# Performance work log

Hardware: AMD Instinct MI355X
Metric: run time of the kernel (lower is better)

Reference implementation:

```python
import jax, jax.numpy as jnp
import numpy as np

B, T, D, F, E = 4, 2048, 1024, 2048, 16  # batch, seq, hidden, intermediate, experts


def setup_inputs() -> dict:
    key = jax.random.key(0)
    k0, k1, k2, k3 = jax.random.split(key, 4)
    x = jax.random.normal(k0, (B, T, D), dtype=jnp.float32)
    # gate: torch Linear(D, E, bias=False); store as [D, E] so logits = h @ Wg
    Wg = jax.random.normal(k1, (D, E), dtype=jnp.float32) * 0.02
    # experts: kaiming_uniform(a=sqrt(5)) -> U(-1/sqrt(fan_in), 1/sqrt(fan_in))
    W1 = jax.random.uniform(k2, (E, D, F), minval=-1.0, maxval=1.0, dtype=jnp.float32) / np.sqrt(D)
    W2 = jax.random.uniform(k3, (E, F, D), minval=-1.0, maxval=1.0, dtype=jnp.float32) / np.sqrt(F)
    return {"x": x, "Wg": Wg, "W1": W1, "W2": W2}


def reference(x, Wg, W1, W2):
    b, t, d = x.shape
    e = Wg.shape[1]
    h = x.reshape(-1, d)                     # [N, D], N = b*t tokens
    n = h.shape[0]

    # --- gate: top-2 routing with fp32 softmax over the 2 selected logits ---
    logits = h @ Wg                          # [N, E]
    scores, idx = jax.lax.top_k(logits, 2)   # [N, 2]
    scores = jax.nn.softmax(scores.astype(jnp.float32), axis=-1).astype(x.dtype)

    # dense combine weights [N, E]: weight of expert e for each token (0 if not routed)
    combine = jnp.zeros((n, e), dtype=x.dtype).at[
        jnp.arange(n)[:, None], idx
    ].add(scores)

    # --- dispatch/combine: scan over experts, weight-accumulate outputs ---
    # Mathematically identical to the masked-loop original: tokens not routed
    # to expert e contribute with weight 0.
    def step(acc, params):
        W1e, W2e, w = params                  # [D,F], [F,D], [N]
        out = jax.nn.silu(h @ W1e) @ W2e      # [N, D]
        return acc + w[:, None] * out, None

    y, _ = jax.lax.scan(step, jnp.zeros_like(h), (W1, W2, combine.T))
    return y.reshape(b, t, d)
```

## Files before the change

### kernel.cpp

```cpp
#include <hip/hip_runtime.h>
#include <hip/hip_bf16.h>

#define NTOK 8192
#define DDIM 1024
#define FDIM 2048
#define NEXP 16
#define CAP   1280
#define CAPRG 80

#define WS_COUNTS 0
#define WS_TOKL   4096
#define WS_WGTL   (4096 + NTOK*NEXP*4)
#define WS_POS    (4096 + 2*NTOK*NEXP*4)
#define WS_TW     (4096 + 2*NTOK*NEXP*4 + NTOK*8)
#define WS2_XG   (size_t)(2u<<20)
#define WS2_W1   (size_t)(42u<<20)
#define WS2_W2   (size_t)(106u<<20)
#define WS2_UG   (size_t)(170u<<20)

typedef short bf16x8 __attribute__((ext_vector_type(8)));
typedef float f32x4  __attribute__((ext_vector_type(4)));

__device__ __forceinline__ unsigned short f2bf(float f) {
  unsigned int u = __builtin_bit_cast(unsigned int, f);
  u += 0x7fffu + ((u >> 16) & 1u);
  return (unsigned short)(u >> 16);
}
__device__ __forceinline__ unsigned int pk2(float a, float b) {
  return (unsigned int)f2bf(a) | ((unsigned int)f2bf(b) << 16);
}
__device__ __forceinline__ float bf2f(unsigned int u) {
  return __builtin_bit_cast(float, u << 16);
}
__device__ __forceinline__ float silu_f(float s) {
  return s / (1.f + __expf(-s));
}
__device__ __forceinline__ void gld_lds16(const void* g, void* l) {
  __builtin_amdgcn_global_load_lds((const __attribute__((address_space(1))) void*)g,
                                   (__attribute__((address_space(3))) void*)l, 16, 0, 0);
}

__global__ __launch_bounds__(1024) void gate_kernel(
    const float* __restrict__ x, const float* __restrict__ Wg,
    int* __restrict__ counts, int* __restrict__ tokl, float* __restrict__ wgtl,
    int* __restrict__ pos, float* __restrict__ tw) {
  __shared__ float WgT[NEXP][DDIM];
  __shared__ int   se[32];
  __shared__ float swt[32];
  __shared__ int   sbase[16];
  int tid = threadIdx.x;
#pragma unroll
  for (int i = 0; i < 4; ++i) {
    int i4 = i * 1024 + tid;
    float4 v = ((const float4*)Wg)[i4];
    int k = i4 >> 2;
    int e0 = (i4 * 4) & 15;
    WgT[e0][k] = v.x; WgT[e0 + 1][k] = v.y;
    WgT[e0 + 2][k] = v.z; WgT[e0 + 3][k] = v.w;
  }
  __syncthreads();

  int wid = tid >> 6, lane = tid & 63;
  int tok = blockIdx.x * 16 + wid;
  const float* xr = x + (size_t)tok * DDIM;
  float xv[16];
#pragma unroll
  for (int j = 0; j < 16; ++j) xv[j] = xr[lane + 64 * j];
  float lg[NEXP];
#pragma unroll
  for (int e = 0; e < NEXP; ++e) {
    float s = 0.f;
#pragma unroll
    for (int j = 0; j < 16; ++j) s += xv[j] * WgT[e][lane + 64 * j];
#pragma unroll
    for (int off = 32; off > 0; off >>= 1) s += __shfl_xor(s, off);
    lg[e] = s;
  }
  int e0 = 0; float b0 = lg[0];
#pragma unroll
  for (int e = 1; e < NEXP; ++e) if (lg[e] > b0) { b0 = lg[e]; e0 = e; }
  int e1 = -1; float b1 = -3.4e38f;
#pragma unroll
  for (int e = 0; e < NEXP; ++e) if (e != e0 && lg[e] > b1) { b1 = lg[e]; e1 = e; }
  float t = expf(b1 - b0);
  float w0 = 1.f / (1.f + t);
  float w1 = t / (1.f + t);
  if (lane == 0) {
    se[wid * 2] = e0;  swt[wid * 2] = w0;
    se[wid * 2 + 1] = e1;  swt[wid * 2 + 1] = w1;
  }
  __syncthreads();

  if (tid < 16) {
    int cnt = 0;
#pragma unroll
    for (int i = 0; i < 32; ++i) cnt += (se[i] == tid) ? 1 : 0;
    sbase[tid] = cnt ? atomicAdd(&counts[tid * 16], cnt) : 0;
    int slot = sbase[tid];
    for (int i = 0; i < 32; ++i) {
      if (se[i] == tid) {
        int tk = blockIdx.x * 16 + (i >> 1);
        float w = swt[i];
        if (slot < CAP) { tokl[tid * NTOK + slot] = tk; wgtl[tid * NTOK + slot] = w; }
        pos[tk * 2 + (i & 1)] = (slot < CAP) ? (tid * CAP + slot) : -1;
        tw[tk * 2 + (i & 1)] = w;
        slot++;
      }
    }
  }
}

__global__ __launch_bounds__(256) void convert_w2(
    const float* __restrict__ W1, const float* __restrict__ W2,
    unsigned short* __restrict__ W1s, unsigned short* __restrict__ W2s) {
  __shared__ float tile[32][133];
  int b = blockIdx.x;
  bool isw2 = b >= 8192;
  int bb = isw2 ? b - 8192 : b;
  int e = bb >> 9;
  int r = bb & 511;
  int t = threadIdx.x;
  const float* src;
  int kk, cb, C;
  if (!isw2) {
    kk = r >> 4; cb = r & 15; C = FDIM;
    src = W1 + ((size_t)e << 21) + (size_t)(kk * 32) * FDIM + cb * 128;
  } else {
    kk = r >> 3; cb = r & 7; C = DDIM;
    src = W2 + ((size_t)e << 21) + (size_t)(kk * 32) * DDIM + cb * 128;
  }
  int c4 = (t & 31) * 4, rr0 = t >> 5;
#pragma unroll
  for (int rd = 0; rd < 4; ++rd) {
    int rr = rr0 + rd * 8;
    float4 v = *(const float4*)(src + (size_t)rr * C + c4);
    tile[rr][c4] = v.x; tile[rr][c4 + 1] = v.y;
    tile[rr][c4 + 2] = v.z; tile[rr][c4 + 3] = v.w;
  }
  __syncthreads();
  int w = t >> 6, lane = t & 63, llo = lane & 15, lhi = lane >> 4;
#pragma unroll
  for (int u = 0; u < 2; ++u) {
    int c2 = w * 2 + u;
    float v[8];
#pragma unroll
    for (int j = 0; j < 8; ++j) {
      int row = isw2 ? (4 * lhi + (j & 3) + 16 * (j >> 2)) : (lhi * 8 + j);
      v[j] = tile[row][c2 * 16 + llo];
    }
    uint4 o;
    o.x = pk2(v[0], v[1]); o.y = pk2(v[2], v[3]);
    o.z = pk2(v[4], v[5]); o.w = pk2(v[6], v[7]);
    size_t gid = isw2 ? (((size_t)e * 64 + kk) * 64 + (cb * 8 + c2))
                      : (((size_t)e * 128 + (cb * 8 + c2)) * 32 + kk);
    *(uint4*)((isw2 ? W2s : W1s) + (gid << 9) + lane * 8) = o;
  }
}

__global__ __launch_bounds__(512) void gather_x(
    const float* __restrict__ x, const int* __restrict__ counts,
    const int* __restrict__ tokl, unsigned short* __restrict__ Xg) {
  int chunk = blockIdx.x * 8 + (threadIdx.x >> 6);
  int lane = threadIdx.x & 63, llo = lane & 15, lhi = lane >> 4;
  int kb = chunk & 31;
  int rg = (chunk >> 5) % CAPRG;
  int e = chunk / (CAPRG * 32);
  int cnt = min(counts[e * 16], CAP);
  int slot = rg * 16 + llo;
  uint4 o = {0u, 0u, 0u, 0u};
  if (slot < cnt) {
    int tok = tokl[e * NTOK + slot];
    const float* p = x + (size_t)tok * DDIM + kb * 32 + lhi * 8;
    float4 a = *(const float4*)p, b2 = *(const float4*)(p + 4);
    o.x = pk2(a.x, a.y); o.y = pk2(a.z, a.w);
    o.z = pk2(b2.x, b2.y); o.w = pk2(b2.z, b2.w);
  }
  *(uint4*)(Xg + ((size_t)chunk << 9) + lane * 8) = o;
}

__global__ __launch_bounds__(512, 2) void g1(
    const unsigned short* __restrict__ W1s, const unsigned short* __restrict__ Xg,
    const int* __restrict__ counts, unsigned short* __restrict__ Ug) {
  int id = blockIdx.x;
  int xcd = id & 7, q = id >> 3;
  int r = q / 40, s = q % 40;
  int e = xcd * 2 + r;
  int ft = s & 7;
  int tt = s >> 3;
  int cnt = min(counts[e * 16], CAP);
  if (tt * 256 >= cnt) return;

  extern __shared__ char smem[];
  int tid = threadIdx.x, wid = tid >> 6, lane = tid & 63;
  int llo = lane & 15, lhi = lane >> 4;
  int wm = wid >> 2, wn = wid & 3;

  f32x4 acc[8][4];
#pragma unroll
  for (int i = 0; i < 8; ++i)
#pragma unroll
    for (int j = 0; j < 4; ++j) acc[i][j] = (f32x4){0.f, 0.f, 0.f, 0.f};

  const size_t abase = ((size_t)e * 128 + ft * 16) * 32;
  const size_t bbase = ((size_t)e * CAPRG + tt * 16) * 32;

#define G1_STAGE(B, T)                                                          \
  {                                                                             \
    char* dst = smem + (B) * 65536;                                             \
    _Pragma("unroll")                                                           \
    for (int i = 0; i < 8; ++i) {                                               \
      int c = wid * 8 + i;                                                      \
      if (c < 32) {                                                             \
        int fl = c >> 1, kkl = c & 1;                                           \
        gld_lds16(W1s + ((abase + (size_t)fl * 32 + (T) * 2 + kkl) << 9) + lane * 8, \
                  dst + c * 1024);                                              \
      } else {                                                                  \
        int cb = c - 32, rgl = cb >> 1, kkl = cb & 1;                           \
        gld_lds16(Xg + ((bbase + (size_t)rgl * 32 + (T) * 2 + kkl) << 9) + lane * 8, \
                  dst + c * 1024);                                              \
      }                                                                         \
    }                                                                           \
  }

  G1_STAGE(0, 0);
  int cur = 0;
  for (int t = 0; t < 16; ++t) {
    if (t < 15) {
      G1_STAGE(cur ^ 1, t + 1);
      asm volatile("s_waitcnt vmcnt(8)" ::: "memory");
    } else {
      asm volatile("s_waitcnt vmcnt(0)" ::: "memory");
    }
    __builtin_amdgcn_s_barrier();
    const char* bufc = smem + cur * 65536;
#pragma unroll
    for (int kk = 0; kk < 2; ++kk) {
      bf16x8 af[8], bx[4];
#pragma unroll
      for (int fi = 0; fi < 8; ++fi)
        af[fi] = *(const bf16x8*)(bufc + (((wm * 8 + fi) * 2 + kk) << 10) + lane * 16);
#pragma unroll
      for (int ti = 0; ti < 4; ++ti)
        bx[ti] = *(const bf16x8*)(bufc + 32768 + (((wn * 4 + ti) * 2 + kk) << 10) + lane * 16);
#pragma unroll
      for (int fi = 0; fi < 8; ++fi)
#pragma unroll
        for (int ti = 0; ti < 4; ++ti)
          acc[fi][ti] = __builtin_amdgcn_mfma_f32_16x16x32_bf16(af[fi], bx[ti], acc[fi][ti], 0, 0, 0);
    }
    asm volatile("s_waitcnt lgkmcnt(0)" ::: "memory");
    __builtin_amdgcn_s_barrier();
    cur ^= 1;
  }

#pragma unroll
  for (int ti = 0; ti < 4; ++ti) {
    int rg = tt * 16 + wn * 4 + ti;
#pragma unroll
    for (int p = 0; p < 4; ++p) {
      int fo = ft * 8 + wm * 4 + p;
      uint4 v;
      v.x = pk2(silu_f(acc[2 * p][ti][0]), silu_f(acc[2 * p][ti][1]));
      v.y = pk2(silu_f(acc[2 * p][ti][2]), silu_f(acc[2 * p][ti][3]));
      v.z = pk2(silu_f(acc[2 * p + 1][ti][0]), silu_f(acc[2 * p + 1][ti][1]));
      v.w = pk2(silu_f(acc[2 * p + 1][ti][2]), silu_f(acc[2 * p + 1][ti][3]));
      *(uint4*)(Ug + ((((size_t)e * CAPRG + rg) * 64 + fo) << 9) + lane * 8) = v;
    }
  }
}

__global__ __launch_bounds__(512, 2) void g2(
    const unsigned short* __restrict__ W2s, const unsigned short* __restrict__ Ug,
    const int* __restrict__ counts, unsigned short* __restrict__ Yp) {
  int id = blockIdx.x;
  int xcd = id & 7, q = id >> 3;
  int r = q / 20, s = q % 20;
  int e = xcd * 2 + r;
  int dt = s & 3;
  int tt = s >> 2;
  int cnt = min(counts[e * 16], CAP);
  int tb0 = tt * 256;
  if (tb0 >= cnt) return;

  extern __shared__ char smem[];
  int tid = threadIdx.x;
  int wid = tid >> 6, lane = tid & 63, llo = lane & 15, lhi = lane >> 4;
  int wm = wid >> 2, wn = wid & 3;

  f32x4 acc[8][4];
#pragma unroll
  for (int i = 0; i < 8; ++i)
#pragma unroll
    for (int j = 0; j < 4; ++j) acc[i][j] = (f32x4){0.f, 0.f, 0.f, 0.f};

  const size_t abase = (size_t)e * 4096 + dt * 16;
  const size_t bbase = ((size_t)e * CAPRG + tt * 16) * 64;

#define G2_STAGE(B, T)                                                          \
  {                                                                             \
    char* dst = smem + (B) * 65536;                                             \
    _Pragma("unroll")                                                           \
    for (int i = 0; i < 8; ++i) {                                               \
      int c = wid * 8 + i;                                                      \
      if (c < 32) {                                                             \
        int cl = c >> 1, kkl = c & 1;                                           \
        gld_lds16(W2s + ((abase + (size_t)((T) * 2 + kkl) * 64 + cl) << 9) + lane * 8, \
                  dst + c * 1024);                                              \
      } else {                                                                  \
        int cb = c - 32, rgl = cb >> 1, kkl = cb & 1;                           \
        gld_lds16(Ug + ((bbase + (size_t)rgl * 64 + (T) * 2 + kkl) << 9) + lane * 8, \
                  dst + c * 1024);                                              \
      }                                                                         \
    }                                                                           \
  }

  G2_STAGE(0, 0);
  int cur = 0;
  for (int t = 0; t < 32; ++t) {
    if (t < 31) {
      G2_STAGE(cur ^ 1, t + 1);
      asm volatile("s_waitcnt vmcnt(8)" ::: "memory");
    } else {
      asm volatile("s_waitcnt vmcnt(0)" ::: "memory");
    }
    __builtin_amdgcn_s_barrier();
    const char* bufc = smem + cur * 65536;
#pragma unroll
    for (int kk = 0; kk < 2; ++kk) {
      bf16x8 aw[8], bu[4];
#pragma unroll
      for (int di = 0; di < 8; ++di)
        aw[di] = *(const bf16x8*)(bufc + (((wm * 8 + di) * 2 + kk) << 10) + lane * 16);
#pragma unroll
      for (int ti = 0; ti < 4; ++ti)
        bu[ti] = *(const bf16x8*)(bufc + 32768 + (((wn * 4 + ti) * 2 + kk) << 10) + lane * 16);
#pragma unroll
      for (int di = 0; di < 8; ++di)
#pragma unroll
        for (int ti = 0; ti < 4; ++ti)
          acc[di][ti] = __builtin_amdgcn_mfma_f32_16x16x32_bf16(aw[di], bu[ti], acc[di][ti], 0, 0, 0);
    }
    asm volatile("s_waitcnt lgkmcnt(0)" ::: "memory");
    __builtin_amdgcn_s_barrier();
    cur ^= 1;
  }

#pragma unroll
  for (int di = 0; di < 8; ++di)
#pragma unroll
    for (int ti = 0; ti < 4; ++ti) {
      int slot = tb0 + wn * 64 + ti * 16 + llo;
      int d = dt * 256 + wm * 128 + di * 16 + 4 * lhi;
      uint2 v;
      v.x = pk2(acc[di][ti][0], acc[di][ti][1]);
      v.y = pk2(acc[di][ti][2], acc[di][ti][3]);
      *(uint2*)(Yp + (((size_t)e * CAP + slot) << 10) + d) = v;
    }
}

__global__ __launch_bounds__(256) void combine_k(
    const unsigned short* __restrict__ Yp, const int* __restrict__ pos,
    const float* __restrict__ tw, float* __restrict__ out) {
  int gid = blockIdx.x * 256 + threadIdx.x;
  int tok = gid >> 7, oct = gid & 127;
  int p0 = pos[tok * 2], p1 = pos[tok * 2 + 1];
  float w0 = tw[tok * 2], w1 = tw[tok * 2 + 1];
  float r[8];
#pragma unroll
  for (int j = 0; j < 8; ++j) r[j] = 0.f;
  if (p0 >= 0) {
    uint4 a = *(const uint4*)(Yp + (((size_t)p0) << 10) + (oct << 3));
    unsigned int w[4] = {a.x, a.y, a.z, a.w};
#pragma unroll
    for (int h = 0; h < 4; ++h) {
      r[2 * h]     += w0 * bf2f(w[h] & 0xffffu);
      r[2 * h + 1] += w0 * bf2f(w[h] >> 16);
    }
  }
  if (p1 >= 0) {
    uint4 a = *(const uint4*)(Yp + (((size_t)p1) << 10) + (oct << 3));
    unsigned int w[4] = {a.x, a.y, a.z, a.w};
#pragma unroll
    for (int h = 0; h < 4; ++h) {
      r[2 * h]     += w1 * bf2f(w[h] & 0xffffu);
      r[2 * h + 1] += w1 * bf2f(w[h] >> 16);
    }
  }
  float4 o0 = {r[0], r[1], r[2], r[3]}, o1 = {r[4], r[5], r[6], r[7]};
  float* dst = out + ((size_t)tok << 10) + (oct << 3);
  *(float4*)dst = o0;
  *(float4*)(dst + 4) = o1;
}

extern "C" void kernel_launch(void* const* d_in, const int* in_sizes, int n_in,
                              void* d_out, int out_size, void* d_ws, size_t ws_size,
                              hipStream_t stream) {
  const float* x  = (const float*)d_in[0];
  const float* Wg = (const float*)d_in[1];
  const float* W1 = (const float*)d_in[2];
  const float* W2 = (const float*)d_in[3];
  float* out = (float*)d_out;

  int*   counts = (int*)((char*)d_ws + WS_COUNTS);
  int*   tokl   = (int*)((char*)d_ws + WS_TOKL);
  float* wgtl   = (float*)((char*)d_ws + WS_WGTL);
  int*   pos    = (int*)((char*)d_ws + WS_POS);
  float* tw     = (float*)((char*)d_ws + WS_TW);
  unsigned short* XgN = (unsigned short*)((char*)d_ws + WS2_XG);
  unsigned short* W1n = (unsigned short*)((char*)d_ws + WS2_W1);
  unsigned short* W2n = (unsigned short*)((char*)d_ws + WS2_W2);
  unsigned short* UgN = (unsigned short*)((char*)d_ws + WS2_UG);

  hipMemsetAsync(counts, 0, 1024, stream);

  gate_kernel<<<NTOK / 16, 1024, 0, stream>>>(x, Wg, counts, tokl, wgtl, pos, tw);
  convert_w2<<<16384, 256, 0, stream>>>(W1, W2, W1n, W2n);
  gather_x<<<5120, 512, 0, stream>>>(x, counts, tokl, XgN);

  hipFuncSetAttribute((const void*)g1,
                      hipFuncAttributeMaxDynamicSharedMemorySize, 131072);
  hipFuncSetAttribute((const void*)g2,
                      hipFuncAttributeMaxDynamicSharedMemorySize, 131072);
  g1<<<NEXP * 8 * 5, 512, 131072, stream>>>(W1n, XgN, counts, UgN);
  g2<<<NEXP * 4 * 5, 512, 131072, stream>>>(W2n, UgN, counts, XgN );
  combine_k<<<4096, 256, 0, stream>>>(XgN , pos, tw, out);
}
```

Baseline: 373.9 us.

## Interleave LDS reads, global prefetch and MFMA in four phases per k-step

Result: slower. 410.0 us (+9.6%).

```diff
diff --git a/kernel.cpp b/kernel.cpp
--- a/kernel.cpp
+++ b/kernel.cpp
@@ -204,51 +204,83 @@
   const size_t abase = ((size_t)e * 128 + ft * 16) * 32;
   const size_t bbase = ((size_t)e * CAPRG + tt * 16) * 32;
 
-#define G1_STAGE(B, T)                                                          \
+#define G1_STAGE2(DST, T, P)                                                    \
   {                                                                             \
-    char* dst = smem + (B) * 65536;                                             \
-    _Pragma("unroll")                                                           \
-    for (int i = 0; i < 8; ++i) {                                               \
-      int c = wid * 8 + i;                                                      \
+    _Pragma("unroll")                                                           \
+    for (int i2 = 2 * (P); i2 < 2 * (P) + 2; ++i2) {                            \
+      int c = wid * 8 + i2;                                                     \
       if (c < 32) {                                                             \
         int fl = c >> 1, kkl = c & 1;                                           \
         gld_lds16(W1s + ((abase + (size_t)fl * 32 + (T) * 2 + kkl) << 9) + lane * 8, \
-                  dst + c * 1024);                                              \
+                  (DST) + c * 1024);                                            \
       } else {                                                                  \
         int cb = c - 32, rgl = cb >> 1, kkl = cb & 1;                           \
         gld_lds16(Xg + ((bbase + (size_t)rgl * 32 + (T) * 2 + kkl) << 9) + lane * 8, \
-                  dst + c * 1024);                                              \
+                  (DST) + c * 1024);                                            \
       }                                                                         \
     }                                                                           \
   }
 
-  G1_STAGE(0, 0);
+  {
+    char* d0 = smem;
+    G1_STAGE2(d0, 0, 0); G1_STAGE2(d0, 0, 1); G1_STAGE2(d0, 0, 2); G1_STAGE2(d0, 0, 3);
+  }
+  asm volatile("s_waitcnt vmcnt(0)" ::: "memory");
+  __builtin_amdgcn_s_barrier();
+
   int cur = 0;
   for (int t = 0; t < 16; ++t) {
-    if (t < 15) {
-      G1_STAGE(cur ^ 1, t + 1);
-      asm volatile("s_waitcnt vmcnt(8)" ::: "memory");
-    } else {
-      asm volatile("s_waitcnt vmcnt(0)" ::: "memory");
-    }
-    __builtin_amdgcn_s_barrier();
     const char* bufc = smem + cur * 65536;
-#pragma unroll
-    for (int kk = 0; kk < 2; ++kk) {
-      bf16x8 af[8], bx[4];
-#pragma unroll
-      for (int fi = 0; fi < 8; ++fi)
-        af[fi] = *(const bf16x8*)(bufc + (((wm * 8 + fi) * 2 + kk) << 10) + lane * 16);
-#pragma unroll
-      for (int ti = 0; ti < 4; ++ti)
-        bx[ti] = *(const bf16x8*)(bufc + 32768 + (((wn * 4 + ti) * 2 + kk) << 10) + lane * 16);
-#pragma unroll
-      for (int fi = 0; fi < 8; ++fi)
-#pragma unroll
-        for (int ti = 0; ti < 4; ++ti)
-          acc[fi][ti] = __builtin_amdgcn_mfma_f32_16x16x32_bf16(af[fi], bx[ti], acc[fi][ti], 0, 0, 0);
-    }
-    asm volatile("s_waitcnt lgkmcnt(0)" ::: "memory");
+    char* dstn = smem + (cur ^ 1) * 65536;
+    bool pf = (t < 15);
+    bf16x8 af[4], bx[4];
+
+#define G1_LD_AF(FB, KK)                                                        \
+    _Pragma("unroll")                                                           \
+    for (int fi = 0; fi < 4; ++fi)                                              \
+      af[fi] = *(const bf16x8*)(bufc + (((wm * 8 + (FB) + fi) * 2 + (KK)) << 10) + lane * 16);
+#define G1_LD_BX(KK)                                                            \
+    _Pragma("unroll")                                                           \
+    for (int ti = 0; ti < 4; ++ti)                                              \
+      bx[ti] = *(const bf16x8*)(bufc + 32768 + (((wn * 4 + ti) * 2 + (KK)) << 10) + lane * 16);
+#define G1_MFMA(FB)                                                             \
+    __builtin_amdgcn_s_setprio(1);                                              \
+    _Pragma("unroll")                                                           \
+    for (int fi = 0; fi < 4; ++fi)                                              \
+      _Pragma("unroll")                                                         \
+      for (int ti = 0; ti < 4; ++ti)                                            \
+        acc[(FB) + fi][ti] =                                                    \
+            __builtin_amdgcn_mfma_f32_16x16x32_bf16(af[fi], bx[ti], acc[(FB) + fi][ti], 0, 0, 0); \
+    __builtin_amdgcn_s_setprio(0);
+
+    G1_LD_AF(0, 0) G1_LD_BX(0)
+    if (pf) G1_STAGE2(dstn, t + 1, 0);
+    __builtin_amdgcn_s_barrier();
+    asm volatile("s_waitcnt lgkmcnt(0)" ::: "memory");
+    __builtin_amdgcn_sched_barrier(0);
+    G1_MFMA(0)
+    __builtin_amdgcn_s_barrier();
+    G1_LD_AF(4, 0)
+    if (pf) G1_STAGE2(dstn, t + 1, 1);
+    __builtin_amdgcn_s_barrier();
+    asm volatile("s_waitcnt lgkmcnt(0)" ::: "memory");
+    __builtin_amdgcn_sched_barrier(0);
+    G1_MFMA(4)
+    __builtin_amdgcn_s_barrier();
+    G1_LD_AF(0, 1) G1_LD_BX(1)
+    if (pf) G1_STAGE2(dstn, t + 1, 2);
+    __builtin_amdgcn_s_barrier();
+    asm volatile("s_waitcnt lgkmcnt(0)" ::: "memory");
+    __builtin_amdgcn_sched_barrier(0);
+    G1_MFMA(0)
+    __builtin_amdgcn_s_barrier();
+    G1_LD_AF(4, 1)
+    if (pf) G1_STAGE2(dstn, t + 1, 3);
+    __builtin_amdgcn_s_barrier();
+    asm volatile("s_waitcnt lgkmcnt(0)" ::: "memory");
+    __builtin_amdgcn_sched_barrier(0);
+    G1_MFMA(4)
+    asm volatile("s_waitcnt vmcnt(0)" ::: "memory");
     __builtin_amdgcn_s_barrier();
     cur ^= 1;
   }
@@ -296,51 +328,86 @@
   const size_t abase = (size_t)e * 4096 + dt * 16;
   const size_t bbase = ((size_t)e * CAPRG + tt * 16) * 64;
 
-#define G2_STAGE(B, T)                                                          \
+#define G2_STAGE2(DST, T, P)                                                    \
   {                                                                             \
-    char* dst = smem + (B) * 65536;                                             \
-    _Pragma("unroll")                                                           \
-    for (int i = 0; i < 8; ++i) {                                               \
-      int c = wid * 8 + i;                                                      \
+    _Pragma("unroll")                                                           \
+    for (int i2 = 2 * (P); i2 < 2 * (P) + 2; ++i2) {                            \
+      int c = wid * 8 + i2;                                                     \
       if (c < 32) {                                                             \
         int cl = c >> 1, kkl = c & 1;                                           \
         gld_lds16(W2s + ((abase + (size_t)((T) * 2 + kkl) * 64 + cl) << 9) + lane * 8, \
-                  dst + c * 1024);                                              \
+                  (DST) + c * 1024);                                            \
       } else {                                                                  \
         int cb = c - 32, rgl = cb >> 1, kkl = cb & 1;                           \
         gld_lds16(Ug + ((bbase + (size_t)rgl * 64 + (T) * 2 + kkl) << 9) + lane * 8, \
-                  dst + c * 1024);                                              \
+                  (DST) + c * 1024);                                            \
       }                                                                         \
     }                                                                           \
   }
 
-  G2_STAGE(0, 0);
+  {
+    char* d0 = smem;
+    G2_STAGE2(d0, 0, 0); G2_STAGE2(d0, 0, 1); G2_STAGE2(d0, 0, 2); G2_STAGE2(d0, 0, 3);
+  }
+  asm volatile("s_waitcnt vmcnt(0)" ::: "memory");
+  __builtin_amdgcn_s_barrier();
+
   int cur = 0;
   for (int t = 0; t < 32; ++t) {
-    if (t < 31) {
-      G2_STAGE(cur ^ 1, t + 1);
-      asm volatile("s_waitcnt vmcnt(8)" ::: "memory");
-    } else {
-      asm volatile("s_waitcnt vmcnt(0)" ::: "memory");
-    }
-    __builtin_amdgcn_s_barrier();
     const char* bufc = smem + cur * 65536;
-#pragma unroll
-    for (int kk = 0; kk < 2; ++kk) {
-      bf16x8 aw[8], bu[4];
-#pragma unroll
-      for (int di = 0; di < 8; ++di)
-        aw[di] = *(const bf16x8*)(bufc + (((wm * 8 + di) * 2 + kk) << 10) + lane * 16);
-#pragma unroll
-      for (int ti = 0; ti < 4; ++ti)
-        bu[ti] = *(const bf16x8*)(bufc + 32768 + (((wn * 4 + ti) * 2 + kk) << 10) + lane * 16);
-#pragma unroll
-      for (int di = 0; di < 8; ++di)
-#pragma unroll
-        for (int ti = 0; ti < 4; ++ti)
-          acc[di][ti] = __builtin_amdgcn_mfma_f32_16x16x32_bf16(aw[di], bu[ti], acc[di][ti], 0, 0, 0);
-    }
-    asm volatile("s_waitcnt lgkmcnt(0)" ::: "memory");
+    char* dstn = smem + (cur ^ 1) * 65536;
+    bool pf = (t < 31);
+    bf16x8 aw[4], bu[4];
+
+#define G2_LD_AW(DB, KK)                                                        \
+    _Pragma("unroll")                                                           \
+    for (int di = 0; di < 4; ++di)                                              \
+      aw[di] = *(const bf16x8*)(bufc + (((wm * 8 + (DB) + di) * 2 + (KK)) << 10) + lane * 16);
+#define G2_LD_BU(KK)                                                            \
+    _Pragma("unroll")                                                           \
+    for (int ti = 0; ti < 4; ++ti)                                              \
+      bu[ti] = *(const bf16x8*)(bufc + 32768 + (((wn * 4 + ti) * 2 + (KK)) << 10) + lane * 16);
+#define G2_MFMA(DB)                                                             \
+    __builtin_amdgcn_s_setprio(1);                                              \
+    _Pragma("unroll")                                                           \
+    for (int di = 0; di < 4; ++di)                                              \
+      _Pragma("unroll")                                                         \
+      for (int ti = 0; ti < 4; ++ti)                                            \
+        acc[(DB) + di][ti] =                                                    \
+            __builtin_amdgcn_mfma_f32_16x16x32_bf16(aw[di], bu[ti], acc[(DB) + di][ti], 0, 0, 0); \
+    __builtin_amdgcn_s_setprio(0);
+
+    G2_LD_AW(0, 0) G2_LD_BU(0)
+    if (pf) G2_STAGE2(dstn, t + 1, 0);
+    __builtin_amdgcn_s_barrier();
+    asm volatile("s_waitcnt lgkmcnt(0)" ::: "memory");
+    __builtin_amdgcn_sched_barrier(0);
+    G2_MFMA(0)
+    __builtin_amdgcn_s_barrier();
+
+    G2_LD_AW(4, 0)
+    if (pf) G2_STAGE2(dstn, t + 1, 1);
+    __builtin_amdgcn_s_barrier();
+    asm volatile("s_waitcnt lgkmcnt(0)" ::: "memory");
+    __builtin_amdgcn_sched_barrier(0);
+    G2_MFMA(4)
+    __builtin_amdgcn_s_barrier();
+
+    G2_LD_AW(0, 1) G2_LD_BU(1)
+    if (pf) G2_STAGE2(dstn, t + 1, 2);
+    __builtin_amdgcn_s_barrier();
+    asm volatile("s_waitcnt lgkmcnt(0)" ::: "memory");
+    __builtin_amdgcn_sched_barrier(0);
+    G2_MFMA(0)
+    __builtin_amdgcn_s_barrier();
+
+    G2_LD_AW(4, 1)
+    if (pf) G2_STAGE2(dstn, t + 1, 3);
+    __builtin_amdgcn_s_barrier();
+    asm volatile("s_waitcnt lgkmcnt(0)" ::: "memory");
+    __builtin_amdgcn_sched_barrier(0);
+    G2_MFMA(4)
+    asm volatile("s_waitcnt vmcnt(0)" ::: "memory");
     __builtin_amdgcn_s_barrier();
     cur ^= 1;
   }
```
